# Optimization experiments

Measured on AMD Instinct MI355X. Metric: run time of the kernel, lower is better.

The kernel has to match this reference:

```python
import jax, jax.numpy as jnp
import numpy as np
import math

B, T, DIM, H = 2, 2048, 1024, 16
HD = DIM // H


def setup_inputs() -> dict:
    key = jax.random.key(0)
    ks = jax.random.split(key, 5)
    s = 1.0 / math.sqrt(DIM)
    return {
        "x": jax.random.normal(ks[0], (B, T, DIM), dtype=jnp.float32),
        "wq": jax.random.normal(ks[1], (DIM, DIM), dtype=jnp.float32) * s,
        "wk": jax.random.normal(ks[2], (DIM, DIM), dtype=jnp.float32) * s,
        "wv": jax.random.normal(ks[3], (DIM, DIM), dtype=jnp.float32) * s,
        "wo": jax.random.normal(ks[4], (DIM, DIM), dtype=jnp.float32) * s,
    }


def reference(x, wq, wk, wv, wo):
    Bc, Tc, C = x.shape
    # nn.Linear applies x @ W.T; weights here stored as [out, in]
    def proj(w):
        return (x @ w.T).reshape(Bc, Tc, H, HD).transpose(0, 2, 1, 3)  # [B,H,T,hd]
    q, k, v = proj(wq), proj(wk), proj(wv)
    scores = jnp.einsum("bhqd,bhkd->bhqk", q, k) / math.sqrt(HD)
    causal = jnp.tril(jnp.ones((Tc, Tc), dtype=bool))
    scores = jnp.where(causal, scores, -jnp.inf)
    attn = jax.nn.softmax(scores, axis=-1)
    out = jnp.einsum("bhqk,bhkd->bhqd", attn, v)
    out = out.transpose(0, 2, 1, 3).reshape(Bc, Tc, C)
    return out @ wo.T
```

## Files before the change

kernel.cpp:

```cpp
#include <hip/hip_runtime.h>
#include <stdint.h>


#define T_SEQ 2048

typedef unsigned short u16;
typedef __attribute__((ext_vector_type(8))) __bf16 bf16x8;
typedef __attribute__((ext_vector_type(4))) float  f32x4;

#define NEG_BIG (-30000.0f)

__device__ __forceinline__ u16 f2bf(float x) {
    union { float f; unsigned u; } c; c.f = x;
    return (u16)((c.u + 0x7fffu + ((c.u >> 16) & 1u)) >> 16);
}

__device__ __forceinline__ void gload_lds16(const void* g, void* l) {
    __builtin_amdgcn_global_load_lds(
        (const __attribute__((address_space(1))) void*)g,
        (__attribute__((address_space(3))) void*)l, 16, 0, 0);
}

__device__ __forceinline__ void storeC(u16* p, float v)   { *p = f2bf(v); }
__device__ __forceinline__ void storeC(float* p, float v) { *p = v; }

__global__ __launch_bounds__(256) void cvt_f32_bf16(
    const float* __restrict__ src, u16* __restrict__ dst, int n4)
{
    int i = blockIdx.x * 256 + threadIdx.x;
    if (i < n4) {
        float4 v = ((const float4*)src)[i];
        ushort4 o;
        o.x = f2bf(v.x); o.y = f2bf(v.y); o.z = f2bf(v.z); o.w = f2bf(v.w);
        ((ushort4*)dst)[i] = o;
    }
}

template <typename OutT, bool VT_MODE>
__global__ __launch_bounds__(256) void gemm_bt(
    const u16* __restrict__ A, const u16* __restrict__ Wb,
    OutT* __restrict__ C0, OutT* __restrict__ C1, OutT* __restrict__ C2)
{
    __shared__ __align__(16) char As[128 * 128];
    __shared__ __align__(16) char Bs[128 * 128];

    const u16* W = Wb + (size_t)blockIdx.z * 1048576u;
    OutT* Cz = blockIdx.z == 0 ? C0 : (blockIdx.z == 1 ? C1 : C2);

    const int tid = threadIdx.x;
    const int w = tid >> 6, l = tid & 63;
    const int wy = w >> 1, wx = w & 1;
    const int bm = blockIdx.y * 128, bn = blockIdx.x * 128;

    f32x4 acc[4][4];
#pragma unroll
    for (int m = 0; m < 4; m++)
#pragma unroll
        for (int n = 0; n < 4; n++) acc[m][n] = (f32x4){0.f, 0.f, 0.f, 0.f};

    const int lrow = l >> 3, lslot = l & 7;

    for (int kt = 0; kt < 16; ++kt) {
#pragma unroll
        for (int c = 0; c < 4; ++c) {
            int ch = w * 4 + c;
            int row = ch * 8 + lrow;
            gload_lds16((const char*)A + ((size_t)(bm + row) * 1024 + kt * 64) * 2 + lslot * 16,
                        As + ch * 1024);
            gload_lds16((const char*)W + ((size_t)(bn + row) * 1024 + kt * 64) * 2 + lslot * 16,
                        Bs + ch * 1024);
        }
        __syncthreads();

#pragma unroll
        for (int kk = 0; kk < 2; ++kk) {
            const int cb = (kk * 32 + (l >> 4) * 8) * 2;
            bf16x8 af[4], bfr[4];
#pragma unroll
            for (int m = 0; m < 4; m++)
                af[m] = *(const bf16x8*)(As + (wy * 64 + m * 16 + (l & 15)) * 128 + cb);
#pragma unroll
            for (int n = 0; n < 4; n++)
                bfr[n] = *(const bf16x8*)(Bs + (wx * 64 + n * 16 + (l & 15)) * 128 + cb);
#pragma unroll
            for (int m = 0; m < 4; m++)
#pragma unroll
                for (int n = 0; n < 4; n++)
                    acc[m][n] = __builtin_amdgcn_mfma_f32_16x16x32_bf16(
                        af[m], bfr[n], acc[m][n], 0, 0, 0);
        }
        __syncthreads();
    }

    const bool vtw = VT_MODE && (blockIdx.z == 2);
#pragma unroll
    for (int m = 0; m < 4; m++) {
        int grow0 = bm + wy * 64 + m * 16 + (l >> 4) * 4;
#pragma unroll
        for (int n = 0; n < 4; n++) {
            int gcol = bn + wx * 64 + n * 16 + (l & 15);
            if (vtw) {
                int bh = (grow0 >> 11) * 16 + (gcol >> 6);
                size_t rowbase = ((size_t)bh * 64 + (gcol & 63)) * T_SEQ + (grow0 & 2047);
#pragma unroll
                for (int r = 0; r < 4; r++)
                    storeC(&Cz[rowbase + r], acc[m][n][r]);
            } else {
#pragma unroll
                for (int r = 0; r < 4; r++)
                    storeC(&Cz[(size_t)(grow0 + r) * 1024 + gcol], acc[m][n][r]);
            }
        }
    }
}

__global__ __launch_bounds__(64) void attn_fwd(
    const u16* __restrict__ Q, const u16* __restrict__ K,
    const u16* __restrict__ VT, u16* __restrict__ O)
{
    __shared__ __align__(16) u16 Ps[16][72];

    const int bh = blockIdx.x;
    const int y = blockIdx.y;
    const int b = bh >> 4, h = bh & 15;
    const int l = threadIdx.x;
    const size_t base = (size_t)b * T_SEQ * 1024 + h * 64;
    const u16* vtb = VT + (size_t)bh * 64 * T_SEQ;

    const int qg = y * 16;
    const int qrow = qg + (l & 15);
    const u16* qp = Q + base + (size_t)qrow * 1024 + (l >> 4) * 8;
    bf16x8 qf[2];
    qf[0] = *(const bf16x8*)(qp);
    qf[1] = *(const bf16x8*)(qp + 32);

    f32x4 oacc[4];
#pragma unroll
    for (int n = 0; n < 4; n++) oacc[n] = (f32x4){0.f, 0.f, 0.f, 0.f};
    float mrun[4], lrun[4];
#pragma unroll
    for (int r = 0; r < 4; r++) { mrun[r] = NEG_BIG; lrun[r] = 0.f; }

    const int ktmax = (qg + 15) >> 6;

    for (int kt = 0; kt <= ktmax; ++kt) {
        f32x4 s[4];
#pragma unroll
        for (int n = 0; n < 4; n++) s[n] = (f32x4){0.f, 0.f, 0.f, 0.f};
#pragma unroll
        for (int kk = 0; kk < 2; ++kk) {
#pragma unroll
            for (int nt = 0; nt < 4; ++nt) {
                if (kt * 64 + nt * 16 <= qg + 15) {
                    bf16x8 kf = *(const bf16x8*)(K + base
                        + (size_t)(kt * 64 + nt * 16 + (l & 15)) * 1024
                        + kk * 32 + (l >> 4) * 8);
                    s[nt] = __builtin_amdgcn_mfma_f32_16x16x32_bf16(qf[kk], kf, s[nt], 0, 0, 0);
                }
            }
        }

        const int jb = kt * 64 + (l & 15);
#pragma unroll
        for (int r = 0; r < 4; ++r) {
            const int qrow_g = qg + (l >> 4) * 4 + r;
            float mt = NEG_BIG;
#pragma unroll
            for (int nt = 0; nt < 4; ++nt) {
                float v = (jb + nt * 16 > qrow_g) ? NEG_BIG : s[nt][r] * 0.125f;
                s[nt][r] = v;
                mt = fmaxf(mt, v);
            }
#pragma unroll
            for (int d = 1; d < 16; d <<= 1) mt = fmaxf(mt, __shfl_xor(mt, d));
            float mnew = fmaxf(mrun[r], mt);
            float alpha = __expf(mrun[r] - mnew);
            mrun[r] = mnew;
            float rs = 0.f;
#pragma unroll
            for (int nt = 0; nt < 4; ++nt) {
                float p = __expf(s[nt][r] - mnew);
                s[nt][r] = p;
                rs += p;
            }
#pragma unroll
            for (int d = 1; d < 16; d <<= 1) rs += __shfl_xor(rs, d);
            lrun[r] = lrun[r] * alpha + rs;
#pragma unroll
            for (int nt = 0; nt < 4; ++nt) oacc[nt][r] *= alpha;
        }

#pragma unroll
        for (int nt = 0; nt < 4; ++nt)
#pragma unroll
            for (int r = 0; r < 4; ++r)
                Ps[(l >> 4) * 4 + r][nt * 16 + (l & 15)] = f2bf(s[nt][r]);

#pragma unroll
        for (int kk = 0; kk < 2; ++kk) {
            if (kt * 64 + kk * 32 <= qg + 15) {
                bf16x8 pf = *(const bf16x8*)(&Ps[l & 15][kk * 32 + (l >> 4) * 8]);
#pragma unroll
                for (int nt = 0; nt < 4; ++nt) {
                    bf16x8 vf = *(const bf16x8*)(vtb
                        + (size_t)(nt * 16 + (l & 15)) * T_SEQ
                        + kt * 64 + kk * 32 + (l >> 4) * 8);
                    oacc[nt] = __builtin_amdgcn_mfma_f32_16x16x32_bf16(pf, vf, oacc[nt], 0, 0, 0);
                }
            }
        }
    }

#pragma unroll
    for (int nt = 0; nt < 4; ++nt) {
        int gcol = h * 64 + nt * 16 + (l & 15);
#pragma unroll
        for (int r = 0; r < 4; ++r) {
            int row = qg + (l >> 4) * 4 + r;
            O[(size_t)b * T_SEQ * 1024 + (size_t)row * 1024 + gcol] = f2bf(oacc[nt][r] / lrun[r]);
        }
    }
}

extern "C" void kernel_launch(void* const* d_in, const int* in_sizes, int n_in,
                              void* d_out, int out_size, void* d_ws, size_t ws_size,
                              hipStream_t stream)
{
    (void)in_sizes; (void)n_in; (void)out_size; (void)ws_size;
    const float* x  = (const float*)d_in[0];
    const float* wq = (const float*)d_in[1];
    const float* wk = (const float*)d_in[2];
    const float* wv = (const float*)d_in[3];
    const float* wo = (const float*)d_in[4];
    float* out = (float*)d_out;

    char* ws = (char*)d_ws;
    u16* xb = (u16*)(ws);
    u16* wb = (u16*)(ws + (8u << 20));
    u16* Kb = (u16*)(ws + (16u << 20));
    u16* VT = (u16*)(ws + (24u << 20));
    u16* Ob = (u16*)(ws + (32u << 20));
    u16* Qb = (u16*)d_out;

    dim3 blk(256);
    cvt_f32_bf16<<<4096, blk, 0, stream>>>(x, xb, 1048576);
    cvt_f32_bf16<<<1024, blk, 0, stream>>>(wq, wb + 0u * 1048576u, 262144);
    cvt_f32_bf16<<<1024, blk, 0, stream>>>(wk, wb + 1u * 1048576u, 262144);
    cvt_f32_bf16<<<1024, blk, 0, stream>>>(wv, wb + 2u * 1048576u, 262144);
    cvt_f32_bf16<<<1024, blk, 0, stream>>>(wo, wb + 3u * 1048576u, 262144);

    gemm_bt<u16, true><<<dim3(8, 32, 3), blk, 0, stream>>>(xb, wb, Qb, Kb, VT);
    attn_fwd<<<dim3(32, 128, 1), dim3(64), 0, stream>>>(Qb, Kb, VT, Ob);
    gemm_bt<float, false><<<dim3(8, 32, 1), blk, 0, stream>>>(Ob, wb + 3u * 1048576u,
                                                              out, out, out);
}
```

Measured before the change: 312.6 us.

## Fuse input conversions, fold softmax scale into Q, transpose attention MFMA layout

Merges the five f32-to-bf16 conversion launches into one kernel. Folds the 1/sqrt(d)*log2(e) scale into the Q projection epilogue so attention can use exp2 directly. Swaps the MFMA operand order so each lane holds one query row, which removes the per-row shuffle reductions, masks only the diagonal tile, and skips rescaling when the max grows by less than a threshold. It also reorders query tiles to balance causal work across blocks and vectorizes the P and O stores. The lazy rescale bound and the scale folded into bf16 Q slightly change numerics.

New measurement: 343.7 us. 10.0% more time.

```diff
diff --git a/kernel.cpp b/kernel.cpp
--- a/kernel.cpp
+++ b/kernel.cpp
@@ -3,6 +3,7 @@
 
 
 #define T_SEQ 2048
+#define QSCALE 0.1803368801111204f
 
 typedef unsigned short u16;
 typedef __attribute__((ext_vector_type(8))) __bf16 bf16x8;
@@ -24,16 +25,25 @@
 __device__ __forceinline__ void storeC(u16* p, float v)   { *p = f2bf(v); }
 __device__ __forceinline__ void storeC(float* p, float v) { *p = v; }
 
-__global__ __launch_bounds__(256) void cvt_f32_bf16(
-    const float* __restrict__ src, u16* __restrict__ dst, int n4)
+__global__ __launch_bounds__(256) void cvt_all(
+    const float* __restrict__ x,  const float* __restrict__ wq,
+    const float* __restrict__ wk, const float* __restrict__ wv,
+    const float* __restrict__ wo, u16* __restrict__ xb, u16* __restrict__ wb)
 {
     int i = blockIdx.x * 256 + threadIdx.x;
-    if (i < n4) {
-        float4 v = ((const float4*)src)[i];
-        ushort4 o;
-        o.x = f2bf(v.x); o.y = f2bf(v.y); o.z = f2bf(v.z); o.w = f2bf(v.w);
-        ((ushort4*)dst)[i] = o;
-    }
+    const float* s; u16* d; int off;
+    if (i < 1048576) { s = x; d = xb; off = i; }
+    else {
+        int j = i - 1048576;
+        int wsel = j >> 18;
+        off = j & 262143;
+        s = wsel == 0 ? wq : wsel == 1 ? wk : wsel == 2 ? wv : wo;
+        d = wb + (size_t)wsel * 1048576u;
+    }
+    float4 v = ((const float4*)s)[off];
+    ushort4 o;
+    o.x = f2bf(v.x); o.y = f2bf(v.y); o.z = f2bf(v.z); o.w = f2bf(v.w);
+    ((ushort4*)d)[off] = o;
 }
 
 template <typename OutT, bool VT_MODE>
@@ -93,6 +103,7 @@
     }
 
     const bool vtw = VT_MODE && (blockIdx.z == 2);
+    const float osc = (VT_MODE && blockIdx.z == 0) ? QSCALE : 1.0f;
 #pragma unroll
     for (int m = 0; m < 4; m++) {
         int grow0 = bm + wy * 64 + m * 16 + (l >> 4) * 4;
@@ -108,7 +119,7 @@
             } else {
 #pragma unroll
                 for (int r = 0; r < 4; r++)
-                    storeC(&Cz[(size_t)(grow0 + r) * 1024 + gcol], acc[m][n][r]);
+                    storeC(&Cz[(size_t)(grow0 + r) * 1024 + gcol], acc[m][n][r] * osc);
             }
         }
     }
@@ -122,14 +133,17 @@
 
     const int bh = blockIdx.x;
     const int y = blockIdx.y;
+    const int qt = (y & 1) ? (127 - (y >> 1)) : (y >> 1);
     const int b = bh >> 4, h = bh & 15;
     const int l = threadIdx.x;
+    const int g = l >> 4, q16 = l & 15;
     const size_t base = (size_t)b * T_SEQ * 1024 + h * 64;
     const u16* vtb = VT + (size_t)bh * 64 * T_SEQ;
 
-    const int qg = y * 16;
-    const int qrow = qg + (l & 15);
-    const u16* qp = Q + base + (size_t)qrow * 1024 + (l >> 4) * 8;
+    const int qg = qt * 16;
+    const int qrow_g = qg + q16;
+
+    const u16* qp = Q + base + (size_t)qrow_g * 1024 + g * 8;
     bf16x8 qf[2];
     qf[0] = *(const bf16x8*)(qp);
     qf[1] = *(const bf16x8*)(qp + 32);
@@ -137,13 +151,13 @@
     f32x4 oacc[4];
 #pragma unroll
     for (int n = 0; n < 4; n++) oacc[n] = (f32x4){0.f, 0.f, 0.f, 0.f};
-    float mrun[4], lrun[4];
-#pragma unroll
-    for (int r = 0; r < 4; r++) { mrun[r] = NEG_BIG; lrun[r] = 0.f; }
+    float mrun = NEG_BIG, lrun = 0.f;
 
     const int ktmax = (qg + 15) >> 6;
 
     for (int kt = 0; kt <= ktmax; ++kt) {
+        const bool diag = (kt == ktmax);
+
         f32x4 s[4];
 #pragma unroll
         for (int n = 0; n < 4; n++) s[n] = (f32x4){0.f, 0.f, 0.f, 0.f};
@@ -153,72 +167,88 @@
             for (int nt = 0; nt < 4; ++nt) {
                 if (kt * 64 + nt * 16 <= qg + 15) {
                     bf16x8 kf = *(const bf16x8*)(K + base
-                        + (size_t)(kt * 64 + nt * 16 + (l & 15)) * 1024
-                        + kk * 32 + (l >> 4) * 8);
-                    s[nt] = __builtin_amdgcn_mfma_f32_16x16x32_bf16(qf[kk], kf, s[nt], 0, 0, 0);
+                        + (size_t)(kt * 64 + nt * 16 + q16) * 1024
+                        + kk * 32 + g * 8);
+                    s[nt] = __builtin_amdgcn_mfma_f32_16x16x32_bf16(kf, qf[kk], s[nt], 0, 0, 0);
                 }
             }
         }
 
-        const int jb = kt * 64 + (l & 15);
-#pragma unroll
-        for (int r = 0; r < 4; ++r) {
-            const int qrow_g = qg + (l >> 4) * 4 + r;
-            float mt = NEG_BIG;
-#pragma unroll
-            for (int nt = 0; nt < 4; ++nt) {
-                float v = (jb + nt * 16 > qrow_g) ? NEG_BIG : s[nt][r] * 0.125f;
-                s[nt][r] = v;
-                mt = fmaxf(mt, v);
-            }
-#pragma unroll
-            for (int d = 1; d < 16; d <<= 1) mt = fmaxf(mt, __shfl_xor(mt, d));
-            float mnew = fmaxf(mrun[r], mt);
-            float alpha = __expf(mrun[r] - mnew);
-            mrun[r] = mnew;
-            float rs = 0.f;
-#pragma unroll
-            for (int nt = 0; nt < 4; ++nt) {
-                float p = __expf(s[nt][r] - mnew);
+        if (diag) {
+#pragma unroll
+            for (int nt = 0; nt < 4; ++nt)
+#pragma unroll
+                for (int r = 0; r < 4; ++r) {
+                    int kg = kt * 64 + nt * 16 + g * 4 + r;
+                    if (kg > qrow_g) s[nt][r] = NEG_BIG;
+                }
+        }
+
+        float pm = s[0][0];
+#pragma unroll
+        for (int nt = 0; nt < 4; ++nt)
+#pragma unroll
+            for (int r = 0; r < 4; ++r) pm = fmaxf(pm, s[nt][r]);
+        pm = fmaxf(pm, __shfl_xor(pm, 16));
+        pm = fmaxf(pm, __shfl_xor(pm, 32));
+
+        const bool noresc = __all(pm <= mrun + 8.0f);
+        float mnew = noresc ? mrun : fmaxf(mrun, pm);
+
+        float rs = 0.f;
+#pragma unroll
+        for (int nt = 0; nt < 4; ++nt)
+#pragma unroll
+            for (int r = 0; r < 4; ++r) {
+                float p = __builtin_amdgcn_exp2f(s[nt][r] - mnew);
                 s[nt][r] = p;
                 rs += p;
             }
-#pragma unroll
-            for (int d = 1; d < 16; d <<= 1) rs += __shfl_xor(rs, d);
-            lrun[r] = lrun[r] * alpha + rs;
-#pragma unroll
-            for (int nt = 0; nt < 4; ++nt) oacc[nt][r] *= alpha;
-        }
-
-#pragma unroll
-        for (int nt = 0; nt < 4; ++nt)
-#pragma unroll
-            for (int r = 0; r < 4; ++r)
-                Ps[(l >> 4) * 4 + r][nt * 16 + (l & 15)] = f2bf(s[nt][r]);
+        rs += __shfl_xor(rs, 16);
+        rs += __shfl_xor(rs, 32);
+
+        if (!noresc) {
+            float alpha = __builtin_amdgcn_exp2f(mrun - mnew);
+            lrun *= alpha;
+#pragma unroll
+            for (int nt = 0; nt < 4; ++nt)
+#pragma unroll
+                for (int r = 0; r < 4; ++r) oacc[nt][r] *= alpha;
+            mrun = mnew;
+        }
+        lrun += rs;
+
+#pragma unroll
+        for (int nt = 0; nt < 4; ++nt) {
+            ushort4 pk;
+            pk.x = f2bf(s[nt][0]); pk.y = f2bf(s[nt][1]);
+            pk.z = f2bf(s[nt][2]); pk.w = f2bf(s[nt][3]);
+            *(ushort4*)(&Ps[q16][nt * 16 + g * 4]) = pk;
+        }
 
 #pragma unroll
         for (int kk = 0; kk < 2; ++kk) {
             if (kt * 64 + kk * 32 <= qg + 15) {
-                bf16x8 pf = *(const bf16x8*)(&Ps[l & 15][kk * 32 + (l >> 4) * 8]);
+                bf16x8 pf = *(const bf16x8*)(&Ps[q16][kk * 32 + g * 8]);
 #pragma unroll
                 for (int nt = 0; nt < 4; ++nt) {
                     bf16x8 vf = *(const bf16x8*)(vtb
-                        + (size_t)(nt * 16 + (l & 15)) * T_SEQ
-                        + kt * 64 + kk * 32 + (l >> 4) * 8);
-                    oacc[nt] = __builtin_amdgcn_mfma_f32_16x16x32_bf16(pf, vf, oacc[nt], 0, 0, 0);
+                        + (size_t)(nt * 16 + q16) * T_SEQ
+                        + kt * 64 + kk * 32 + g * 8);
+                    oacc[nt] = __builtin_amdgcn_mfma_f32_16x16x32_bf16(vf, pf, oacc[nt], 0, 0, 0);
                 }
             }
         }
     }
 
+    const float rinv = __builtin_amdgcn_rcpf(lrun);
+    u16* orow = O + (size_t)b * T_SEQ * 1024 + (size_t)(qg + q16) * 1024 + h * 64;
 #pragma unroll
     for (int nt = 0; nt < 4; ++nt) {
-        int gcol = h * 64 + nt * 16 + (l & 15);
-#pragma unroll
-        for (int r = 0; r < 4; ++r) {
-            int row = qg + (l >> 4) * 4 + r;
-            O[(size_t)b * T_SEQ * 1024 + (size_t)row * 1024 + gcol] = f2bf(oacc[nt][r] / lrun[r]);
-        }
+        ushort4 ov;
+        ov.x = f2bf(oacc[nt][0] * rinv); ov.y = f2bf(oacc[nt][1] * rinv);
+        ov.z = f2bf(oacc[nt][2] * rinv); ov.w = f2bf(oacc[nt][3] * rinv);
+        *(ushort4*)(orow + nt * 16 + g * 4) = ov;
     }
 }
 
@@ -243,11 +273,7 @@
     u16* Qb = (u16*)d_out;
 
     dim3 blk(256);
-    cvt_f32_bf16<<<4096, blk, 0, stream>>>(x, xb, 1048576);
-    cvt_f32_bf16<<<1024, blk, 0, stream>>>(wq, wb + 0u * 1048576u, 262144);
-    cvt_f32_bf16<<<1024, blk, 0, stream>>>(wk, wb + 1u * 1048576u, 262144);
-    cvt_f32_bf16<<<1024, blk, 0, stream>>>(wv, wb + 2u * 1048576u, 262144);
-    cvt_f32_bf16<<<1024, blk, 0, stream>>>(wo, wb + 3u * 1048576u, 262144);
+    cvt_all<<<8192, blk, 0, stream>>>(x, wq, wk, wv, wo, xb, wb);
 
     gemm_bt<u16, true><<<dim3(8, 32, 3), blk, 0, stream>>>(xb, wb, Qb, Kb, VT);
     attn_fwd<<<dim3(32, 128, 1), dim3(64), 0, stream>>>(Qb, Kb, VT, Ob);
```
